# Kernel tuning notes

Measured on AMD Instinct MI355X. Metric: run time of the kernel, lower is better.

Reference implementation:

```python
import jax, jax.numpy as jnp
import numpy as np

D = 128        # node_state_dim
F = 10         # len(CHOSEN_CONNECTION_FEATURES)
N_IP = 20000
N_CONN = 100000
E = 200000
T = 3


def _seg_mean(vals, ids, n):
    s = jax.ops.segment_sum(vals, ids, num_segments=n)
    c = jax.ops.segment_sum(jnp.ones((vals.shape[0], 1), vals.dtype), ids, num_segments=n)
    return s / jnp.maximum(c, 1.0)


def _gru(x, h, kernel, rec_kernel, bias):
    # keras GRUCell, reset_after=True, gate order [z, r, hh]
    xm = x @ kernel + bias[0]
    hm = h @ rec_kernel + bias[1]
    xz, xr, xh = jnp.split(xm, 3, axis=-1)
    hz, hr, hh = jnp.split(hm, 3, axis=-1)
    z = jax.nn.sigmoid(xz + hz)
    r = jax.nn.sigmoid(xr + hr)
    hcand = jnp.tanh(xh + r * hh)
    return z * h + (1.0 - z) * hcand


def setup_inputs() -> dict:
    key = jax.random.key(0)
    ks = jax.random.split(key, 24)
    s = 0.02
    inp = {
        "feature_connection": jax.random.normal(ks[0], (N_CONN, F), jnp.float32),
        "src_ip_to_connection": jax.random.randint(ks[1], (E,), 0, N_IP, jnp.int32),
        "dst_ip_to_connection": jax.random.randint(ks[2], (E,), 0, N_CONN, jnp.int32),
        "src_connection_to_ip": jax.random.randint(ks[3], (E,), 0, N_CONN, jnp.int32),
        "dst_connection_to_ip": jax.random.randint(ks[4], (E,), 0, N_IP, jnp.int32),
        # message MLPs
        "W_m1": jax.random.normal(ks[5], (2 * D, D), jnp.float32) * s,
        "b_m1": jnp.zeros((D,), jnp.float32),
        "W_m2": jax.random.normal(ks[6], (2 * D, D), jnp.float32) * s,
        "b_m2": jnp.zeros((D,), jnp.float32),
        # GRU cells
        "gru_ip_k": jax.random.normal(ks[7], (D, 3 * D), jnp.float32) * s,
        "gru_ip_r": jax.random.normal(ks[8], (D, 3 * D), jnp.float32) * s,
        "gru_ip_b": jnp.zeros((2, 3 * D), jnp.float32),
        "gru_c_k": jax.random.normal(ks[9], (D, 3 * D), jnp.float32) * s,
        "gru_c_r": jax.random.normal(ks[10], (D, 3 * D), jnp.float32) * s,
        "gru_c_b": jnp.zeros((2, 3 * D), jnp.float32),
        # readout MLP
        "W_r1": jax.random.normal(ks[11], (D, 128), jnp.float32) * s,
        "b_r1": jnp.zeros((128,), jnp.float32),
        "W_r2": jax.random.normal(ks[12], (128, 64), jnp.float32) * s,
        "b_r2": jnp.zeros((64,), jnp.float32),
        "W_r3": jax.random.normal(ks[13], (64, 15), jnp.float32) * s,
        "b_r3": jnp.zeros((15,), jnp.float32),
    }
    return inp


def reference(feature_connection, src_ip_to_connection, dst_ip_to_connection,
              src_connection_to_ip, dst_connection_to_ip,
              W_m1, b_m1, W_m2, b_m2,
              gru_ip_k, gru_ip_r, gru_ip_b,
              gru_c_k, gru_c_r, gru_c_b,
              W_r1, b_r1, W_r2, b_r2, W_r3, b_r3):
    ip_state = jnp.ones((N_IP, D), jnp.float32)
    connection_state = jnp.concatenate(
        [feature_connection, jnp.zeros((N_CONN, D - F), jnp.float32)], axis=1)

    for _ in range(T):
        # ip -> connection messages
        nn_in = jnp.concatenate([ip_state[src_ip_to_connection],
                                 connection_state[dst_ip_to_connection]], axis=1)
        ip_message = jax.nn.relu(nn_in @ W_m1 + b_m1)            # [E, D]
        ip_mean = _seg_mean(ip_message, dst_ip_to_connection, N_CONN)
        # connection -> ip messages
        nn_in2 = jnp.concatenate([connection_state[src_connection_to_ip],
                                  ip_state[dst_connection_to_ip]], axis=1)
        conn_message = jax.nn.relu(nn_in2 @ W_m2 + b_m2)         # [E, D]
        conn_mean = _seg_mean(conn_message, dst_connection_to_ip, N_IP)
        # GRU updates
        ip_state = _gru(conn_mean, ip_state, gru_ip_k, gru_ip_r, gru_ip_b)
        connection_state = _gru(ip_mean, connection_state, gru_c_k, gru_c_r, gru_c_b)

    h = jax.nn.relu(connection_state @ W_r1 + b_r1)
    h = jax.nn.relu(h @ W_r2 + b_r2)
    return jax.nn.softmax(h @ W_r3 + b_r3, axis=-1)              # [N_CONN, 15]
```

## Files before the change

### kernel.cpp

```cpp
#include <hip/hip_runtime.h>
#include <math.h>

#define D 128
#define NF 10
#define N_IP 20000
#define N_CONN 100000
#define NE 200000
#define T_ROUNDS 3

typedef unsigned short u16;
using bf16x8 = __attribute__((ext_vector_type(8))) short;
using floatx4 = __attribute__((ext_vector_type(4))) float;

__device__ inline u16 f2bf(float f) {
  union { float f; unsigned u; } v; v.f = f;
  unsigned u = v.u;
  return (u16)((u + 0x7fffu + ((u >> 16) & 1u)) >> 16);
}
__device__ inline float bf2f(u16 h) {
  union { unsigned u; float f; } v; v.u = ((unsigned)h) << 16; return v.f;
}

__device__ inline float fsigmoid(float s) { return 1.f / (1.f + __expf(-s)); }
__device__ inline float ftanh(float a) {
  a = fminf(fmaxf(a, -15.f), 15.f);
  float e = __expf(2.f * a);
  return (e - 1.f) / (e + 1.f);
}

__device__ __forceinline__ void gld16(const u16* g, u16* l) {
  __builtin_amdgcn_global_load_lds(
      (const __attribute__((address_space(1))) unsigned int*)g,
      (__attribute__((address_space(3))) unsigned int*)l, 16, 0, 0);
}

__global__ void k_init_all(u16* __restrict__ ip_state, u16* __restrict__ conn_state,
                           const float* __restrict__ feat, int* __restrict__ cnt) {
  int i = blockIdx.x * blockDim.x + threadIdx.x;
  const int nip = N_IP * D;
  const int nstate = (N_IP + N_CONN) * D;
  if (i < nip) {
    ip_state[i] = 0x3F80;
  } else if (i < nstate) {
    int j = i - nip;
    int r = j >> 7, c = j & 127;
    conn_state[j] = (c < NF) ? f2bf(feat[r * NF + c]) : (u16)0;
  }
  if (i < N_CONN + N_IP) cnt[i] = 0;
}

__global__ void k_prep_all(
    const float* __restrict__ gik, const float* __restrict__ gir,
    const float* __restrict__ gck, const float* __restrict__ gcr,
    const float* __restrict__ Wm1, const float* __restrict__ Wm2,
    const float* __restrict__ Wr1, const float* __restrict__ Wr2,
    u16* __restrict__ gikb, u16* __restrict__ girb,
    u16* __restrict__ gckb, u16* __restrict__ gcrb,
    u16* __restrict__ wm1b, u16* __restrict__ wm2b,
    u16* __restrict__ wm1t, u16* __restrict__ wm2t,
    u16* __restrict__ wr1b, u16* __restrict__ wr2b, float* __restrict__ csum) {
  int i = blockIdx.x * blockDim.x + threadIdx.x;
  if (i < 196608) {
    int m = i / 49152, r = i % 49152;
    const float* W = (m == 0) ? gik : (m == 1) ? gir : (m == 2) ? gck : gcr;
    u16* Wb = (m == 0) ? gikb : (m == 1) ? girb : (m == 2) ? gckb : gcrb;
    int col = r >> 7, k = r & 127;
    Wb[r] = f2bf(W[k * 384 + col]);
  } else if (i < 278528) {
    int j = i - 196608;
    int m = j / 16384, r = j % 16384;
    const float* W; u16* Wb; int k0;
    if (m == 0) { W = Wm1; Wb = wm1b; k0 = 128; }
    else if (m == 1) { W = Wm2; Wb = wm2b; k0 = 128; }
    else if (m == 2) { W = Wm1; Wb = wm1t; k0 = 0; }
    else if (m == 3) { W = Wm2; Wb = wm2t; k0 = 0; }
    else { W = Wr1; Wb = wr1b; k0 = 0; }
    int col = r >> 7, k = r & 127;
    Wb[r] = f2bf(W[(k0 + k) * 128 + col]);
  } else if (i < 286720) {
    int r = i - 278528;
    int col = r >> 7, k = r & 127;
    wr2b[r] = f2bf(Wr2[k * 64 + col]);
  } else if (i < 286848) {
    int c = i - 286720;
    float s = 0.f;
    for (int k = 0; k < 128; k++) s += Wm1[k * 128 + c];
    csum[c] = s;
  }
}

__global__ void k_initP_count(const float* __restrict__ csum, const float* __restrict__ feat,
                              const float* __restrict__ Wm2,
                              u16* __restrict__ P1, u16* __restrict__ P2,
                              const int* __restrict__ d1, const int* __restrict__ d2,
                              int* __restrict__ c1, int* __restrict__ c2) {
  int i = blockIdx.x * blockDim.x + threadIdx.x;
  if (i < NE) {
    atomicAdd(&c1[d1[i]], 1);
    atomicAdd(&c2[d2[i]], 1);
  }
  const int n1 = N_IP * 16;
  const int n2 = N_CONN * 16;
  if (i < n1) {
    int r = i >> 4, g = i & 15;
    u16 v[8];
#pragma unroll
    for (int k = 0; k < 8; k++) v[k] = f2bf(csum[g * 8 + k]);
    *(uint4*)(P1 + (size_t)r * 128 + g * 8) = *(const uint4*)v;
  } else if (i < n1 + n2) {
    int j = i - n1;
    int r = j >> 4, g = j & 15;
    float acc[8] = {0.f, 0.f, 0.f, 0.f, 0.f, 0.f, 0.f, 0.f};
#pragma unroll
    for (int k = 0; k < NF; k++) {
      float f = feat[(size_t)r * NF + k];
      const float* wrow = Wm2 + (size_t)k * 128 + g * 8;
#pragma unroll
      for (int c = 0; c < 8; c++) acc[c] += f * wrow[c];
    }
    u16 v[8];
#pragma unroll
    for (int c = 0; c < 8; c++) v[c] = f2bf(acc[c]);
    *(uint4*)(P2 + (size_t)r * 128 + g * 8) = *(const uint4*)v;
  }
}

__global__ void k_scan_part2(const int* __restrict__ cnt1, int* __restrict__ bsum1,
                             int n1, int nb1,
                             const int* __restrict__ cnt2, int* __restrict__ bsum2, int n2) {
  const int* cnt; int* bsum; int n, b;
  if ((int)blockIdx.x < nb1) { cnt = cnt1; bsum = bsum1; n = n1; b = blockIdx.x; }
  else { cnt = cnt2; bsum = bsum2; n = n2; b = blockIdx.x - nb1; }
  int t = threadIdx.x;
  int base = b * 1024 + t * 4;
  int s = 0;
#pragma unroll
  for (int i = 0; i < 4; i++) { int j = base + i; if (j < n) s += cnt[j]; }
  for (int d = 32; d > 0; d >>= 1) s += __shfl_xor(s, d, 64);
  __shared__ int wred[4];
  int lane = t & 63, wv = t >> 6;
  if (lane == 0) wred[wv] = s;
  __syncthreads();
  if (t == 0) bsum[b] = wred[0] + wred[1] + wred[2] + wred[3];
}

__device__ inline void scan_mid_body(int* bsum, int m, int t) {
  int v = (t < m) ? bsum[t] : 0;
  int lane = t & 63, wv = t >> 6;
  int x = v;
  for (int d = 1; d < 64; d <<= 1) { int y = __shfl_up(x, d, 64); if (lane >= d) x += y; }
  __shared__ int wsum[4];
  if (lane == 63) wsum[wv] = x;
  __syncthreads();
  int add = 0;
  for (int i = 0; i < wv; i++) add += wsum[i];
  int ex = add + x - v;
  if (t < m) bsum[t] = ex;
  __syncthreads();
}

__global__ void k_scan_mid2(int* __restrict__ bsum1, int m1, int* __restrict__ bsum2, int m2) {
  int t = threadIdx.x;
  scan_mid_body(bsum1, m1, t);
  scan_mid_body(bsum2, m2, t);
}

__global__ void k_scan_final2(const int* __restrict__ cnt1, const int* __restrict__ bsum1,
                              int* __restrict__ off1, int* __restrict__ cur1, int n1, int nb1,
                              const int* __restrict__ cnt2, const int* __restrict__ bsum2,
                              int* __restrict__ off2, int* __restrict__ cur2, int n2) {
  const int* cnt; const int* bsum; int* off; int* cur; int n, b;
  if ((int)blockIdx.x < nb1) {
    cnt = cnt1; bsum = bsum1; off = off1; cur = cur1; n = n1; b = blockIdx.x;
  } else {
    cnt = cnt2; bsum = bsum2; off = off2; cur = cur2; n = n2; b = blockIdx.x - nb1;
  }
  int t = threadIdx.x;
  int base = b * 1024 + t * 4;
  int vals[4]; int s = 0;
#pragma unroll
  for (int i = 0; i < 4; i++) {
    int j = base + i;
    vals[i] = (j < n) ? cnt[j] : 0;
    s += vals[i];
  }
  int lane = t & 63, wv = t >> 6;
  int x = s;
  for (int d = 1; d < 64; d <<= 1) { int y = __shfl_up(x, d, 64); if (lane >= d) x += y; }
  __shared__ int wsum[4];
  if (lane == 63) wsum[wv] = x;
  __syncthreads();
  int add = 0;
  for (int i = 0; i < wv; i++) add += wsum[i];
  int run = add + x - s + bsum[b];
#pragma unroll
  for (int i = 0; i < 4; i++) {
    int j = base + i;
    if (j < n) { off[j] = run; cur[j] = run; }
    run += vals[i];
  }
}

__global__ void k_scatter(const int* __restrict__ s1, const int* __restrict__ d1,
                          const int* __restrict__ s2, const int* __restrict__ d2,
                          int* __restrict__ cur1, int* __restrict__ cur2,
                          int* __restrict__ o1, int* __restrict__ o2) {
  int e = blockIdx.x * blockDim.x + threadIdx.x;
  if (e >= NE) return;
  int p1 = atomicAdd(&cur1[d1[e]], 1);
  o1[p1] = s1[e];
  int p2 = atomicAdd(&cur2[d2[e]], 1);
  o2[p2] = s2[e];
}

__global__ __launch_bounds__(256, 4) void k_msggru(
    u16* __restrict__ st1, const u16* __restrict__ wq1, const float* __restrict__ qb1,
    const u16* __restrict__ P1g, const int* __restrict__ srcs1g,
    const int* __restrict__ off1g, const int* __restrict__ cnt1g,
    const u16* __restrict__ wx1, const u16* __restrict__ wh1, const float* __restrict__ gb1,
    const u16* __restrict__ wp1, u16* __restrict__ Pn1, int r1, int tiles1,
    u16* __restrict__ st2, const u16* __restrict__ wq2, const float* __restrict__ qb2,
    const u16* __restrict__ P2g, const int* __restrict__ srcs2g,
    const int* __restrict__ off2g, const int* __restrict__ cnt2g,
    const u16* __restrict__ wx2, const u16* __restrict__ wh2, const float* __restrict__ gb2,
    const u16* __restrict__ wp2, u16* __restrict__ Pn2, int r2, int doP) {
  __shared__ __align__(16) char smem[40960];
  u16* Wls = (u16*)smem;
  u16* Qb = (u16*)smem;
  u16* bufA = (u16*)smem;
  u16* bufB = (u16*)(smem + 12288);
  u16* Hls = (u16*)(smem + 24576);
  int* offLs = (int*)(smem + 24064);
  int* cntLs = (int*)(smem + 24320);
  u16* H; const u16* Wqb; const float* qbias; const u16* P;
  const int* srcs; const int* off; const int* cnt;
  const u16* Wxb; const u16* Whb; const float* gbias;
  const u16* Wpt; u16* Pn; int rows, bm;
  if ((int)blockIdx.x < tiles1) {
    H = st1; Wqb = wq1; qbias = qb1; P = P1g; srcs = srcs1g; off = off1g; cnt = cnt1g;
    Wxb = wx1; Whb = wh1; gbias = gb1; Wpt = wp1; Pn = Pn1; rows = r1; bm = blockIdx.x * 64;
  } else {
    H = st2; Wqb = wq2; qbias = qb2; P = P2g; srcs = srcs2g; off = off2g; cnt = cnt2g;
    Wxb = wx2; Whb = wh2; gbias = gb2; Wpt = wp2; Pn = Pn2; rows = r2;
    bm = (blockIdx.x - tiles1) * 64;
  }
  const int tid = threadIdx.x, wv = tid >> 6, lane = tid & 63;
  const int lrow = lane & 15, quad = lane >> 4;
  const int slot = lane & 15;
  const int rowl = wv * 4 + (lane >> 4);
#pragma unroll
  for (int i = 0; i < 4; i++)
    gld16(Wqb + (size_t)(i * 16 + rowl) * 128 + ((slot ^ rowl) * 8),
          Wls + (size_t)(i * 16 + wv * 4) * 128 + lane * 8);
#pragma unroll
  for (int i = 0; i < 4; i++)
    gld16(H + (size_t)(bm + i * 16 + rowl) * 128 + ((slot ^ rowl) * 8),
          Hls + (size_t)(i * 16 + wv * 4) * 128 + lane * 8);
  if (tid < 64) {
    int node = bm + tid;
    offLs[tid] = (node < rows) ? off[node] : 0;
    cntLs[tid] = (node < rows) ? cnt[node] : 0;
  }
  __syncthreads();
  bf16x8 ah[4];
#pragma unroll
  for (int ks = 0; ks < 4; ks++)
    ah[ks] = *(const bf16x8*)(Hls + (size_t)(wv * 16 + lrow) * 128 + (((ks * 4 + quad) ^ lrow) * 8));
  floatx4 acc[8];
#pragma unroll
  for (int ct = 0; ct < 8; ct++) acc[ct] = {0.f, 0.f, 0.f, 0.f};
#pragma unroll
  for (int ks = 0; ks < 4; ks++) {
#pragma unroll
    for (int j = 0; j < 4; j++) {
      bf16x8 b = *(const bf16x8*)(Wls + (size_t)(j * 16 + lrow) * 128 + (((4 * ks + quad) ^ lrow) * 8));
      acc[j] = __builtin_amdgcn_mfma_f32_16x16x32_bf16(ah[ks], b, acc[j], 0, 0, 0);
    }
  }
  __syncthreads();
#pragma unroll
  for (int i = 0; i < 4; i++)
    gld16(Wqb + (size_t)(64 + i * 16 + rowl) * 128 + ((slot ^ rowl) * 8),
          Wls + (size_t)(i * 16 + wv * 4) * 128 + lane * 8);
  __syncthreads();
#pragma unroll
  for (int ks = 0; ks < 4; ks++) {
#pragma unroll
    for (int j = 0; j < 4; j++) {
      bf16x8 b = *(const bf16x8*)(Wls + (size_t)(j * 16 + lrow) * 128 + (((4 * ks + quad) ^ lrow) * 8));
      acc[4 + j] = __builtin_amdgcn_mfma_f32_16x16x32_bf16(ah[ks], b, acc[4 + j], 0, 0, 0);
    }
  }
  __syncthreads();
#pragma unroll
  for (int ct = 0; ct < 8; ct++) {
    int col = ct * 16 + lrow;
    float bv = qbias[col];
#pragma unroll
    for (int reg = 0; reg < 4; reg++) {
      int lr = wv * 16 + quad * 4 + reg;
      Qb[(size_t)lr * 128 + col] = f2bf(acc[ct][reg] + bv);
    }
  }
  __syncthreads();
#pragma unroll
  for (int it = 0; it < 4; it++) {
    int task = it * 256 + tid;
    int nl = task >> 4, g = task & 15;
    int node = bm + nl;
    if (node >= rows) continue;
    int c8 = g << 3;
    float q[8];
    {
      uint4 qv = *(const uint4*)(Qb + (size_t)nl * 128 + c8);
      unsigned qq[4] = {qv.x, qv.y, qv.z, qv.w};
#pragma unroll
      for (int k = 0; k < 4; k++) {
        q[2 * k] = __uint_as_float(qq[k] << 16);
        q[2 * k + 1] = __uint_as_float(qq[k] & 0xffff0000u);
      }
    }
    float acg[8] = {0.f, 0.f, 0.f, 0.f, 0.f, 0.f, 0.f, 0.f};
    int o = offLs[nl], n = cntLs[nl];
    int i = 0;
    for (; i + 4 <= n; i += 4) {
      int s0 = srcs[o + i], s1 = srcs[o + i + 1], s2 = srcs[o + i + 2], s3 = srcs[o + i + 3];
      uint4 v0 = *(const uint4*)(P + (size_t)s0 * 128 + c8);
      uint4 v1 = *(const uint4*)(P + (size_t)s1 * 128 + c8);
      uint4 v2 = *(const uint4*)(P + (size_t)s2 * 128 + c8);
      uint4 v3 = *(const uint4*)(P + (size_t)s3 * 128 + c8);
      unsigned w[16] = {v0.x, v0.y, v0.z, v0.w, v1.x, v1.y, v1.z, v1.w,
                        v2.x, v2.y, v2.z, v2.w, v3.x, v3.y, v3.z, v3.w};
#pragma unroll
      for (int e = 0; e < 4; e++)
#pragma unroll
        for (int k = 0; k < 4; k++) {
          unsigned ww = w[e * 4 + k];
          float lo = __uint_as_float(ww << 16);
          float hi = __uint_as_float(ww & 0xffff0000u);
          acg[2 * k] += fmaxf(lo + q[2 * k], 0.f);
          acg[2 * k + 1] += fmaxf(hi + q[2 * k + 1], 0.f);
        }
    }
    for (; i < n; i++) {
      int s0 = srcs[o + i];
      uint4 v0 = *(const uint4*)(P + (size_t)s0 * 128 + c8);
      unsigned w[4] = {v0.x, v0.y, v0.z, v0.w};
#pragma unroll
      for (int k = 0; k < 4; k++) {
        unsigned ww = w[k];
        float lo = __uint_as_float(ww << 16);
        float hi = __uint_as_float(ww & 0xffff0000u);
        acg[2 * k] += fmaxf(lo + q[2 * k], 0.f);
        acg[2 * k + 1] += fmaxf(hi + q[2 * k + 1], 0.f);
      }
    }
    float inv = 1.f / fmaxf((float)n, 1.f);
    bf16x8 ov;
#pragma unroll
    for (int k = 0; k < 8; k++) ov[k] = (short)f2bf(acg[k] * inv);
    *(bf16x8*)(Qb + (size_t)nl * 128 + ((g ^ (nl & 15)) * 8)) = ov;
  }
  __syncthreads();
  bf16x8 ax[4];
#pragma unroll
  for (int ks = 0; ks < 4; ks++)
    ax[ks] = *(const bf16x8*)(Qb + (size_t)(wv * 16 + lrow) * 128 + (((ks * 4 + quad) ^ lrow) * 8));
  const int lr0 = wv * 16 + quad * 4;
  __syncthreads();
#pragma unroll
  for (int j = 0; j < 3; j++)
    gld16(Wxb + (size_t)(j * 128 + 0 * 16 + rowl) * 128 + ((slot ^ rowl) * 8),
          bufA + (size_t)(j * 16 + wv * 4) * 128 + lane * 8);
  for (int ch = 0; ch < 8; ch++) {
    __syncthreads();
#pragma unroll
    for (int j = 0; j < 3; j++)
      gld16(Whb + (size_t)(j * 128 + ch * 16 + rowl) * 128 + ((slot ^ rowl) * 8),
            bufB + (size_t)(j * 16 + wv * 4) * 128 + lane * 8);
    floatx4 gacc[3][2];
#pragma unroll
    for (int g = 0; g < 3; g++) {
      gacc[g][0] = {0.f, 0.f, 0.f, 0.f};
      gacc[g][1] = {0.f, 0.f, 0.f, 0.f};
    }
#pragma unroll
    for (int ks = 0; ks < 4; ks++) {
      int posu = ((4 * ks + quad) ^ lrow) * 8;
#pragma unroll
      for (int g = 0; g < 3; g++) {
        bf16x8 bx = *(const bf16x8*)(bufA + (size_t)(g * 16 + lrow) * 128 + posu);
        gacc[g][0] = __builtin_amdgcn_mfma_f32_16x16x32_bf16(ax[ks], bx, gacc[g][0], 0, 0, 0);
      }
    }
    __syncthreads();
    if (ch < 7) {
#pragma unroll
      for (int j = 0; j < 3; j++)
        gld16(Wxb + (size_t)(j * 128 + (ch + 1) * 16 + rowl) * 128 + ((slot ^ rowl) * 8),
              bufA + (size_t)(j * 16 + wv * 4) * 128 + lane * 8);
    }
#pragma unroll
    for (int ks = 0; ks < 4; ks++) {
      int posu = ((4 * ks + quad) ^ lrow) * 8;
#pragma unroll
      for (int g = 0; g < 3; g++) {
        bf16x8 bh = *(const bf16x8*)(bufB + (size_t)(g * 16 + lrow) * 128 + posu);
        gacc[g][1] = __builtin_amdgcn_mfma_f32_16x16x32_bf16(ah[ks], bh, gacc[g][1], 0, 0, 0);
      }
    }
    int hcol = ch * 16 + lrow;
    float bxz = gbias[hcol];
    float bxr = gbias[128 + hcol];
    float bxh = gbias[256 + hcol];
    float bhz = gbias[384 + hcol];
    float bhr = gbias[384 + 128 + hcol];
    float bhh = gbias[384 + 256 + hcol];
    int ggr = 2 * ch + (lrow >> 3);
    int gel = lrow & 7;
#pragma unroll
    for (int reg = 0; reg < 4; reg++) {
      int lr = lr0 + reg;
      float xz = gacc[0][0][reg] + bxz;
      float xr = gacc[1][0][reg] + bxr;
      float xh = gacc[2][0][reg] + bxh;
      float hz = gacc[0][1][reg] + bhz;
      float hr = gacc[1][1][reg] + bhr;
      float hh = gacc[2][1][reg] + bhh;
      float z = fsigmoid(xz + hz);
      float rr = fsigmoid(xr + hr);
      float hc = ftanh(xh + rr * hh);
      u16* hp = Hls + (size_t)lr * 128 + ((ggr ^ (lr & 15)) * 8) + gel;
      float hold = bf2f(*hp);
      *hp = f2bf(z * hold + (1.f - z) * hc);
    }
  }
  __syncthreads();
#pragma unroll
  for (int i = 0; i < 4; i++) {
    int task = i * 256 + tid;
    int row = task >> 4, g = task & 15;
    int grow = bm + row;
    if (grow < rows)
      *(uint4*)(H + (size_t)grow * 128 + g * 8) =
          *(const uint4*)(Hls + (size_t)row * 128 + ((g ^ (row & 15)) * 8));
  }
  if (!doP) return;
  bf16x8 ah2[4];
#pragma unroll
  for (int ks = 0; ks < 4; ks++)
    ah2[ks] = *(const bf16x8*)(Hls + (size_t)(wv * 16 + lrow) * 128 + (((ks * 4 + quad) ^ lrow) * 8));
#pragma unroll
  for (int i = 0; i < 4; i++)
    gld16(Wpt + (size_t)(i * 16 + rowl) * 128 + ((slot ^ rowl) * 8),
          Wls + (size_t)(i * 16 + wv * 4) * 128 + lane * 8);
  __syncthreads();
#pragma unroll
  for (int ct = 0; ct < 8; ct++) acc[ct] = {0.f, 0.f, 0.f, 0.f};
#pragma unroll
  for (int ks = 0; ks < 4; ks++) {
#pragma unroll
    for (int j = 0; j < 4; j++) {
      bf16x8 b = *(const bf16x8*)(Wls + (size_t)(j * 16 + lrow) * 128 + (((4 * ks + quad) ^ lrow) * 8));
      acc[j] = __builtin_amdgcn_mfma_f32_16x16x32_bf16(ah2[ks], b, acc[j], 0, 0, 0);
    }
  }
  __syncthreads();
#pragma unroll
  for (int i = 0; i < 4; i++)
    gld16(Wpt + (size_t)(64 + i * 16 + rowl) * 128 + ((slot ^ rowl) * 8),
          Wls + (size_t)(i * 16 + wv * 4) * 128 + lane * 8);
  __syncthreads();
#pragma unroll
  for (int ks = 0; ks < 4; ks++) {
#pragma unroll
    for (int j = 0; j < 4; j++) {
      bf16x8 b = *(const bf16x8*)(Wls + (size_t)(j * 16 + lrow) * 128 + (((4 * ks + quad) ^ lrow) * 8));
      acc[4 + j] = __builtin_amdgcn_mfma_f32_16x16x32_bf16(ah2[ks], b, acc[4 + j], 0, 0, 0);
    }
  }
  u16* Cls = Hls;
#pragma unroll
  for (int ct = 0; ct < 8; ct++) {
    int col = ct * 16 + lrow;
#pragma unroll
    for (int reg = 0; reg < 4; reg++) {
      int lr = wv * 16 + quad * 4 + reg;
      Cls[(size_t)lr * 128 + col] = f2bf(acc[ct][reg]);
    }
  }
  __syncthreads();
#pragma unroll
  for (int i = 0; i < 4; i++) {
    int task = i * 256 + tid;
    int row = task >> 4, g = task & 15;
    int grow = bm + row;
    if (grow < rows)
      *(uint4*)(Pn + (size_t)grow * 128 + g * 8) =
          *(const uint4*)(Cls + (size_t)row * 128 + g * 8);
  }
}

__global__ __launch_bounds__(256, 4) void k_readout2(
    const u16* __restrict__ S, const u16* __restrict__ W1b, const float* __restrict__ b1,
    const u16* __restrict__ W2b, const float* __restrict__ b2,
    const float* __restrict__ W3, const float* __restrict__ b3,
    float* __restrict__ out, int M) {
  __shared__ __align__(16) char smem[33792];
  u16* Wls = (u16*)smem;
  u16* H1ls = (u16*)smem;
  u16* W2ls = (u16*)(smem + 17408);
  u16* H2ls = (u16*)smem;
  float* W3ls = (float*)(smem + 9216);
  float* b3ls = (float*)(smem + 9216 + 3840);
  const int tid = threadIdx.x, wv = tid >> 6, lane = tid & 63;
  const int lrow = lane & 15, quad = lane >> 4;
  const int slot = lane & 15;
  const int rowl = wv * 4 + (lane >> 4);
  const int bm = blockIdx.x * 64;
#pragma unroll
  for (int i = 0; i < 8; i++)
    gld16(W1b + (size_t)(i * 16 + rowl) * 128 + ((slot ^ rowl) * 8),
          Wls + (size_t)(i * 16 + wv * 4) * 128 + lane * 8);
  const int arow = bm + wv * 16 + lrow;
  const bool arv = arow < M;
  const bf16x8 zv = {0, 0, 0, 0, 0, 0, 0, 0};
  bf16x8 a[4];
#pragma unroll
  for (int ks = 0; ks < 4; ks++)
    a[ks] = arv ? *(const bf16x8*)(S + (size_t)arow * 128 + quad * 8 + ks * 32) : zv;
  __syncthreads();
  floatx4 acc1[8];
#pragma unroll
  for (int ct = 0; ct < 8; ct++) acc1[ct] = {0.f, 0.f, 0.f, 0.f};
#pragma unroll
  for (int ks = 0; ks < 4; ks++) {
#pragma unroll
    for (int ct = 0; ct < 8; ct++) {
      bf16x8 b = *(const bf16x8*)(Wls + (size_t)(ct * 16 + lrow) * 128 + (((4 * ks + quad) ^ lrow) * 8));
      acc1[ct] = __builtin_amdgcn_mfma_f32_16x16x32_bf16(a[ks], b, acc1[ct], 0, 0, 0);
    }
  }
  __syncthreads();
#pragma unroll
  for (int ct = 0; ct < 8; ct++) {
    int col = ct * 16 + lrow;
    float bv = b1[col];
#pragma unroll
    for (int reg = 0; reg < 4; reg++) {
      int lr = wv * 16 + quad * 4 + reg;
      H1ls[(size_t)lr * 136 + col] = f2bf(fmaxf(acc1[ct][reg] + bv, 0.f));
    }
  }
#pragma unroll
  for (int i = 0; i < 4; i++)
    gld16(W2b + (size_t)(i * 16 + rowl) * 128 + ((slot ^ rowl) * 8),
          W2ls + (size_t)(i * 16 + wv * 4) * 128 + lane * 8);
  __syncthreads();
  bf16x8 a2[4];
#pragma unroll
  for (int ks = 0; ks < 4; ks++)
    a2[ks] = *(const bf16x8*)(H1ls + (size_t)(wv * 16 + lrow) * 136 + quad * 8 + ks * 32);
  floatx4 acc2[4];
#pragma unroll
  for (int ct = 0; ct < 4; ct++) acc2[ct] = {0.f, 0.f, 0.f, 0.f};
#pragma unroll
  for (int ks = 0; ks < 4; ks++) {
#pragma unroll
    for (int ct = 0; ct < 4; ct++) {
      bf16x8 b = *(const bf16x8*)(W2ls + (size_t)(ct * 16 + lrow) * 128 + (((4 * ks + quad) ^ lrow) * 8));
      acc2[ct] = __builtin_amdgcn_mfma_f32_16x16x32_bf16(a2[ks], b, acc2[ct], 0, 0, 0);
    }
  }
  __syncthreads();
#pragma unroll
  for (int ct = 0; ct < 4; ct++) {
    int col = ct * 16 + lrow;
    float bv = b2[col];
#pragma unroll
    for (int reg = 0; reg < 4; reg++) {
      int lr = wv * 16 + quad * 4 + reg;
      H2ls[(size_t)lr * 72 + col] = f2bf(fmaxf(acc2[ct][reg] + bv, 0.f));
    }
  }
  for (int l = tid; l < 960; l += 256) W3ls[l] = W3[l];
  if (tid < 15) b3ls[tid] = b3[tid];
  __syncthreads();
  {
    int col = tid & 15;
    int rb = (tid >> 4) * 4;
    float lg[4] = {0.f, 0.f, 0.f, 0.f};
    if (col < 15) {
      float b3v = b3ls[col];
      lg[0] = b3v; lg[1] = b3v; lg[2] = b3v; lg[3] = b3v;
      for (int k = 0; k < 64; k++) {
        float w = W3ls[k * 15 + col];
#pragma unroll
        for (int r = 0; r < 4; r++)
          lg[r] += bf2f(H2ls[(size_t)(rb + r) * 72 + k]) * w;
      }
    }
#pragma unroll
    for (int r = 0; r < 4; r++) {
      float v = (col < 15) ? lg[r] : -3.0e38f;
      float m = v;
#pragma unroll
      for (int d = 1; d < 16; d <<= 1) m = fmaxf(m, __shfl_xor(m, d, 16));
      float e = (col < 15) ? __expf(lg[r] - m) : 0.f;
      float s = e;
#pragma unroll
      for (int d = 1; d < 16; d <<= 1) s += __shfl_xor(s, d, 16);
      int gr2 = bm + rb + r;
      if (col < 15 && gr2 < M) out[(size_t)gr2 * 15 + col] = e / s;
    }
  }
}

extern "C" void kernel_launch(void* const* d_in, const int* in_sizes, int n_in,
                              void* d_out, int out_size, void* d_ws, size_t ws_size,
                              hipStream_t stream) {
  const float* feat = (const float*)d_in[0];
  const int* src1 = (const int*)d_in[1];
  const int* dst1 = (const int*)d_in[2];
  const int* src2 = (const int*)d_in[3];
  const int* dst2 = (const int*)d_in[4];
  const float* Wm1 = (const float*)d_in[5];
  const float* bm1 = (const float*)d_in[6];
  const float* Wm2 = (const float*)d_in[7];
  const float* bm2 = (const float*)d_in[8];
  const float* gik = (const float*)d_in[9];
  const float* gir = (const float*)d_in[10];
  const float* gib = (const float*)d_in[11];
  const float* gck = (const float*)d_in[12];
  const float* gcr = (const float*)d_in[13];
  const float* gcb = (const float*)d_in[14];
  const float* Wr1 = (const float*)d_in[15];
  const float* br1 = (const float*)d_in[16];
  const float* Wr2 = (const float*)d_in[17];
  const float* br2 = (const float*)d_in[18];
  const float* Wr3 = (const float*)d_in[19];
  const float* br3 = (const float*)d_in[20];
  float* out = (float*)d_out;

  u16* w16 = (u16*)d_ws;
  size_t o = 0;
  u16* ip_state = w16 + o;   o += (size_t)N_IP * D;
  u16* conn_state = w16 + o; o += (size_t)N_CONN * D;
  u16* P1a = w16 + o;        o += (size_t)N_IP * D;
  u16* P2a = w16 + o;        o += (size_t)N_CONN * D;
  u16* P1b = w16 + o;        o += (size_t)N_IP * D;
  u16* P2b = w16 + o;        o += (size_t)N_CONN * D;
  u16* gikb = w16 + o;       o += 49152;
  u16* girb = w16 + o;       o += 49152;
  u16* gckb = w16 + o;       o += 49152;
  u16* gcrb = w16 + o;       o += 49152;
  u16* wm1b = w16 + o;       o += 16384;
  u16* wm2b = w16 + o;       o += 16384;
  u16* wm1t = w16 + o;       o += 16384;
  u16* wm2t = w16 + o;       o += 16384;
  u16* wr1b = w16 + o;       o += 16384;
  u16* wr2b = w16 + o;       o += 8192;
  float* csum = (float*)(w16 + o); o += 256;
  int* ip = (int*)(w16 + o);
  int* cnt1 = ip;  ip += N_CONN;
  int* cnt2 = ip;  ip += N_IP;
  int* off1 = ip;  ip += N_CONN;
  int* off2 = ip;  ip += N_IP;
  int* cur1 = ip;  ip += N_CONN;
  int* cur2 = ip;  ip += N_IP;
  int* srcs1 = ip; ip += NE;
  int* srcs2 = ip; ip += NE;
  int* bsum1 = ip; ip += 256;
  int* bsum2 = ip; ip += 256;

  const int BT = 256;

  const int nstate = (N_IP + N_CONN) * D;
  k_init_all<<<(nstate + BT - 1) / BT, BT, 0, stream>>>(ip_state, conn_state, feat, cnt1);
  k_prep_all<<<(286848 + BT - 1) / BT, BT, 0, stream>>>(
      gik, gir, gck, gcr, Wm1, Wm2, Wr1, Wr2,
      gikb, girb, gckb, gcrb, wm1b, wm2b, wm1t, wm2t, wr1b, wr2b, csum);
  const int nPinit = (N_IP + N_CONN) * 16;
  k_initP_count<<<(nPinit + BT - 1) / BT, BT, 0, stream>>>(
      csum, feat, Wm2, P1a, P2a, dst1, dst2, cnt1, cnt2);

  const int nb1 = (N_CONN + 1023) / 1024, nb2 = (N_IP + 1023) / 1024;
  k_scan_part2<<<nb1 + nb2, 256, 0, stream>>>(cnt1, bsum1, N_CONN, nb1, cnt2, bsum2, N_IP);
  k_scan_mid2<<<1, 256, 0, stream>>>(bsum1, nb1, bsum2, nb2);
  k_scan_final2<<<nb1 + nb2, 256, 0, stream>>>(cnt1, bsum1, off1, cur1, N_CONN, nb1,
                                               cnt2, bsum2, off2, cur2, N_IP);
  k_scatter<<<(NE + BT - 1) / BT, BT, 0, stream>>>(src1, dst1, src2, dst2,
                                                   cur1, cur2, srcs1, srcs2);

  const int t64ip = (N_IP + 63) / 64;
  const int t64cn = (N_CONN + 63) / 64;

  u16* P1buf[2] = {P1a, P1b};
  u16* P2buf[2] = {P2a, P2b};
  for (int t = 0; t < T_ROUNDS; t++) {
    int cu = t & 1, nx = cu ^ 1;
    k_msggru<<<t64ip + t64cn, 256, 0, stream>>>(
        ip_state, wm2b, bm2, P2buf[cu], srcs2, off2, cnt2, gikb, girb, gib,
        wm1t, P1buf[nx], N_IP, t64ip,
        conn_state, wm1b, bm1, P1buf[cu], srcs1, off1, cnt1, gckb, gcrb, gcb,
        wm2t, P2buf[nx], N_CONN, (t < T_ROUNDS - 1) ? 1 : 0);
  }

  k_readout2<<<t64cn, 256, 0, stream>>>(conn_state, wr1b, br1, wr2b, br2,
                                        Wr3, br3, out, N_CONN);
}
```

Measured before the change: 447.4 us.

## Enlarge msggru tiles to 128 rows with 512-thread blocks and predicated gather

The fused message+GRU kernel now processes 128 nodes per block with 8 waves instead of 64 nodes with 4 waves. Each staged weight chunk in LDS is therefore reused across twice as many rows. Per-node offset and count are now held in registers instead of LDS. The gather loop handles the remainder through predication instead of a scalar tail loop, and the readout logits loop reads H2 eight values at a time. The larger LDS footprint (64KB) and block size reduce occupancy and may cut the number of resident blocks per CU.

```diff
diff --git a/kernel.cpp b/kernel.cpp
--- a/kernel.cpp
+++ b/kernel.cpp
@@ -213,7 +213,7 @@
   o2[p2] = s2[e];
 }
 
-__global__ __launch_bounds__(256, 4) void k_msggru(
+__global__ __launch_bounds__(512, 4) void k_msggru(
     u16* __restrict__ st1, const u16* __restrict__ wq1, const float* __restrict__ qb1,
     const u16* __restrict__ P1g, const int* __restrict__ srcs1g,
     const int* __restrict__ off1g, const int* __restrict__ cnt1g,
@@ -224,42 +224,45 @@
     const int* __restrict__ off2g, const int* __restrict__ cnt2g,
     const u16* __restrict__ wx2, const u16* __restrict__ wh2, const float* __restrict__ gb2,
     const u16* __restrict__ wp2, u16* __restrict__ Pn2, int r2, int doP) {
-  __shared__ __align__(16) char smem[40960];
+  __shared__ __align__(16) char smem[65536];
   u16* Wls = (u16*)smem;
   u16* Qb = (u16*)smem;
   u16* bufA = (u16*)smem;
   u16* bufB = (u16*)(smem + 12288);
-  u16* Hls = (u16*)(smem + 24576);
-  int* offLs = (int*)(smem + 24064);
-  int* cntLs = (int*)(smem + 24320);
+  u16* Hls = (u16*)(smem + 32768);
   u16* H; const u16* Wqb; const float* qbias; const u16* P;
   const int* srcs; const int* off; const int* cnt;
   const u16* Wxb; const u16* Whb; const float* gbias;
   const u16* Wpt; u16* Pn; int rows, bm;
   if ((int)blockIdx.x < tiles1) {
     H = st1; Wqb = wq1; qbias = qb1; P = P1g; srcs = srcs1g; off = off1g; cnt = cnt1g;
-    Wxb = wx1; Whb = wh1; gbias = gb1; Wpt = wp1; Pn = Pn1; rows = r1; bm = blockIdx.x * 64;
+    Wxb = wx1; Whb = wh1; gbias = gb1; Wpt = wp1; Pn = Pn1; rows = r1; bm = blockIdx.x * 128;
   } else {
     H = st2; Wqb = wq2; qbias = qb2; P = P2g; srcs = srcs2g; off = off2g; cnt = cnt2g;
     Wxb = wx2; Whb = wh2; gbias = gb2; Wpt = wp2; Pn = Pn2; rows = r2;
-    bm = (blockIdx.x - tiles1) * 64;
+    bm = (blockIdx.x - tiles1) * 128;
   }
   const int tid = threadIdx.x, wv = tid >> 6, lane = tid & 63;
   const int lrow = lane & 15, quad = lane >> 4;
-  const int slot = lane & 15;
-  const int rowl = wv * 4 + (lane >> 4);
-#pragma unroll
-  for (int i = 0; i < 4; i++)
-    gld16(Wqb + (size_t)(i * 16 + rowl) * 128 + ((slot ^ rowl) * 8),
-          Wls + (size_t)(i * 16 + wv * 4) * 128 + lane * 8);
-#pragma unroll
-  for (int i = 0; i < 4; i++)
-    gld16(H + (size_t)(bm + i * 16 + rowl) * 128 + ((slot ^ rowl) * 8),
-          Hls + (size_t)(i * 16 + wv * 4) * 128 + lane * 8);
-  if (tid < 64) {
-    int node = bm + tid;
-    offLs[tid] = (node < rows) ? off[node] : 0;
-    cntLs[tid] = (node < rows) ? cnt[node] : 0;
+#pragma unroll
+  for (int j = 0; j < 2; j++) {
+    int c = j * 512 + tid;
+    int row = c >> 4, sl = c & 15;
+    gld16(Wqb + (size_t)row * 128 + ((sl ^ (row & 15)) * 8), Wls + (size_t)c * 8);
+  }
+#pragma unroll
+  for (int i = 0; i < 4; i++) {
+    int c = i * 512 + tid;
+    int row = c >> 4, sl = c & 15;
+    gld16(H + (size_t)(bm + row) * 128 + ((sl ^ (row & 15)) * 8), Hls + (size_t)c * 8);
+  }
+  int oArr[4], nArr[4];
+#pragma unroll
+  for (int it = 0; it < 4; it++) {
+    int nl = (it * 512 + tid) >> 4;
+    int node = bm + nl;
+    oArr[it] = (node < rows) ? off[node] : 0;
+    nArr[it] = (node < rows) ? cnt[node] : 0;
   }
   __syncthreads();
   bf16x8 ah[4];
@@ -279,9 +282,11 @@
   }
   __syncthreads();
 #pragma unroll
-  for (int i = 0; i < 4; i++)
-    gld16(Wqb + (size_t)(64 + i * 16 + rowl) * 128 + ((slot ^ rowl) * 8),
-          Wls + (size_t)(i * 16 + wv * 4) * 128 + lane * 8);
+  for (int j = 0; j < 2; j++) {
+    int c = j * 512 + tid;
+    int row = c >> 4, sl = c & 15;
+    gld16(Wqb + (size_t)(64 + row) * 128 + ((sl ^ (row & 15)) * 8), Wls + (size_t)c * 8);
+  }
   __syncthreads();
 #pragma unroll
   for (int ks = 0; ks < 4; ks++) {
@@ -305,7 +310,7 @@
   __syncthreads();
 #pragma unroll
   for (int it = 0; it < 4; it++) {
-    int task = it * 256 + tid;
+    int task = it * 512 + tid;
     int nl = task >> 4, g = task & 15;
     int node = bm + nl;
     if (node >= rows) continue;
@@ -321,10 +326,13 @@
       }
     }
     float acg[8] = {0.f, 0.f, 0.f, 0.f, 0.f, 0.f, 0.f, 0.f};
-    int o = offLs[nl], n = cntLs[nl];
-    int i = 0;
-    for (; i + 4 <= n; i += 4) {
-      int s0 = srcs[o + i], s1 = srcs[o + i + 1], s2 = srcs[o + i + 2], s3 = srcs[o + i + 3];
+    int o = oArr[it], n = nArr[it];
+    for (int i = 0; i < n; i += 4) {
+      int rem = n - i;
+      int s0 = srcs[o + i];
+      int s1 = srcs[o + i + (rem > 1 ? 1 : 0)];
+      int s2 = srcs[o + i + (rem > 2 ? 2 : 0)];
+      int s3 = srcs[o + i + (rem > 3 ? 3 : 0)];
       uint4 v0 = *(const uint4*)(P + (size_t)s0 * 128 + c8);
       uint4 v1 = *(const uint4*)(P + (size_t)s1 * 128 + c8);
       uint4 v2 = *(const uint4*)(P + (size_t)s2 * 128 + c8);
@@ -332,27 +340,17 @@
       unsigned w[16] = {v0.x, v0.y, v0.z, v0.w, v1.x, v1.y, v1.z, v1.w,
                         v2.x, v2.y, v2.z, v2.w, v3.x, v3.y, v3.z, v3.w};
 #pragma unroll
-      for (int e = 0; e < 4; e++)
+      for (int e = 0; e < 4; e++) {
+        bool val = (e == 0) || (rem > e);
 #pragma unroll
         for (int k = 0; k < 4; k++) {
           unsigned ww = w[e * 4 + k];
           float lo = __uint_as_float(ww << 16);
           float hi = __uint_as_float(ww & 0xffff0000u);
-          acg[2 * k] += fmaxf(lo + q[2 * k], 0.f);
-          acg[2 * k + 1] += fmaxf(hi + q[2 * k + 1], 0.f);
+          float t0 = fmaxf(lo + q[2 * k], 0.f);
+          float t1 = fmaxf(hi + q[2 * k + 1], 0.f);
+          if (val) { acg[2 * k] += t0; acg[2 * k + 1] += t1; }
         }
-    }
-    for (; i < n; i++) {
-      int s0 = srcs[o + i];
-      uint4 v0 = *(const uint4*)(P + (size_t)s0 * 128 + c8);
-      unsigned w[4] = {v0.x, v0.y, v0.z, v0.w};
-#pragma unroll
-      for (int k = 0; k < 4; k++) {
-        unsigned ww = w[k];
-        float lo = __uint_as_float(ww << 16);
-        float hi = __uint_as_float(ww & 0xffff0000u);
-        acg[2 * k] += fmaxf(lo + q[2 * k], 0.f);
-        acg[2 * k + 1] += fmaxf(hi + q[2 * k + 1], 0.f);
       }
     }
     float inv = 1.f / fmaxf((float)n, 1.f);
@@ -369,15 +367,25 @@
   const int lr0 = wv * 16 + quad * 4;
   __syncthreads();
 #pragma unroll
-  for (int j = 0; j < 3; j++)
-    gld16(Wxb + (size_t)(j * 128 + 0 * 16 + rowl) * 128 + ((slot ^ rowl) * 8),
-          bufA + (size_t)(j * 16 + wv * 4) * 128 + lane * 8);
+  for (int j = 0; j < 2; j++) {
+    int c = j * 512 + tid;
+    if (c < 768) {
+      int gate = c >> 8, colw = (c >> 4) & 15, sl = c & 15;
+      gld16(Wxb + (size_t)(gate * 128 + 0 * 16 + colw) * 128 + ((sl ^ colw) * 8),
+            bufA + (size_t)c * 8);
+    }
+  }
   for (int ch = 0; ch < 8; ch++) {
     __syncthreads();
 #pragma unroll
-    for (int j = 0; j < 3; j++)
-      gld16(Whb + (size_t)(j * 128 + ch * 16 + rowl) * 128 + ((slot ^ rowl) * 8),
-            bufB + (size_t)(j * 16 + wv * 4) * 128 + lane * 8);
+    for (int j = 0; j < 2; j++) {
+      int c = j * 512 + tid;
+      if (c < 768) {
+        int gate = c >> 8, colw = (c >> 4) & 15, sl = c & 15;
+        gld16(Whb + (size_t)(gate * 128 + ch * 16 + colw) * 128 + ((sl ^ colw) * 8),
+              bufB + (size_t)c * 8);
+      }
+    }
     floatx4 gacc[3][2];
 #pragma unroll
     for (int g = 0; g < 3; g++) {
@@ -396,9 +404,14 @@
     __syncthreads();
     if (ch < 7) {
 #pragma unroll
-      for (int j = 0; j < 3; j++)
-        gld16(Wxb + (size_t)(j * 128 + (ch + 1) * 16 + rowl) * 128 + ((slot ^ rowl) * 8),
-              bufA + (size_t)(j * 16 + wv * 4) * 128 + lane * 8);
+      for (int j = 0; j < 2; j++) {
+        int c = j * 512 + tid;
+        if (c < 768) {
+          int gate = c >> 8, colw = (c >> 4) & 15, sl = c & 15;
+          gld16(Wxb + (size_t)(gate * 128 + (ch + 1) * 16 + colw) * 128 + ((sl ^ colw) * 8),
+                bufA + (size_t)c * 8);
+        }
+      }
     }
 #pragma unroll
     for (int ks = 0; ks < 4; ks++) {
@@ -438,8 +451,8 @@
   __syncthreads();
 #pragma unroll
   for (int i = 0; i < 4; i++) {
-    int task = i * 256 + tid;
-    int row = task >> 4, g = task & 15;
+    int c = i * 512 + tid;
+    int row = c >> 4, g = c & 15;
     int grow = bm + row;
     if (grow < rows)
       *(uint4*)(H + (size_t)grow * 128 + g * 8) =
@@ -451,9 +464,11 @@
   for (int ks = 0; ks < 4; ks++)
     ah2[ks] = *(const bf16x8*)(Hls + (size_t)(wv * 16 + lrow) * 128 + (((ks * 4 + quad) ^ lrow) * 8));
 #pragma unroll
-  for (int i = 0; i < 4; i++)
-    gld16(Wpt + (size_t)(i * 16 + rowl) * 128 + ((slot ^ rowl) * 8),
-          Wls + (size_t)(i * 16 + wv * 4) * 128 + lane * 8);
+  for (int j = 0; j < 2; j++) {
+    int c = j * 512 + tid;
+    int row = c >> 4, sl = c & 15;
+    gld16(Wpt + (size_t)row * 128 + ((sl ^ (row & 15)) * 8), Wls + (size_t)c * 8);
+  }
   __syncthreads();
 #pragma unroll
   for (int ct = 0; ct < 8; ct++) acc[ct] = {0.f, 0.f, 0.f, 0.f};
@@ -467,9 +482,11 @@
   }
   __syncthreads();
 #pragma unroll
-  for (int i = 0; i < 4; i++)
-    gld16(Wpt + (size_t)(64 + i * 16 + rowl) * 128 + ((slot ^ rowl) * 8),
-          Wls + (size_t)(i * 16 + wv * 4) * 128 + lane * 8);
+  for (int j = 0; j < 2; j++) {
+    int c = j * 512 + tid;
+    int row = c >> 4, sl = c & 15;
+    gld16(Wpt + (size_t)(64 + row) * 128 + ((sl ^ (row & 15)) * 8), Wls + (size_t)c * 8);
+  }
   __syncthreads();
 #pragma unroll
   for (int ks = 0; ks < 4; ks++) {
@@ -492,8 +509,8 @@
   __syncthreads();
 #pragma unroll
   for (int i = 0; i < 4; i++) {
-    int task = i * 256 + tid;
-    int row = task >> 4, g = task & 15;
+    int c = i * 512 + tid;
+    int row = c >> 4, g = c & 15;
     int grow = bm + row;
     if (grow < rows)
       *(uint4*)(Pn + (size_t)grow * 128 + g * 8) =
@@ -593,11 +610,16 @@
     if (col < 15) {
       float b3v = b3ls[col];
       lg[0] = b3v; lg[1] = b3v; lg[2] = b3v; lg[3] = b3v;
-      for (int k = 0; k < 64; k++) {
-        float w = W3ls[k * 15 + col];
-#pragma unroll
-        for (int r = 0; r < 4; r++)
-          lg[r] += bf2f(H2ls[(size_t)(rb + r) * 72 + k]) * w;
+      for (int k8 = 0; k8 < 64; k8 += 8) {
+        float w[8];
+#pragma unroll
+        for (int j = 0; j < 8; j++) w[j] = W3ls[(k8 + j) * 15 + col];
+#pragma unroll
+        for (int r = 0; r < 4; r++) {
+          bf16x8 hv = *(const bf16x8*)(H2ls + (size_t)(rb + r) * 72 + k8);
+#pragma unroll
+          for (int j = 0; j < 8; j++) lg[r] += bf2f((u16)hv[j]) * w[j];
+        }
       }
     }
 #pragma unroll
@@ -692,16 +714,17 @@
   k_scatter<<<(NE + BT - 1) / BT, BT, 0, stream>>>(src1, dst1, src2, dst2,
                                                    cur1, cur2, srcs1, srcs2);
 
-  const int t64ip = (N_IP + 63) / 64;
+  const int t128ip = (N_IP + 127) / 128;
+  const int t128cn = (N_CONN + 127) / 128;
   const int t64cn = (N_CONN + 63) / 64;
 
   u16* P1buf[2] = {P1a, P1b};
   u16* P2buf[2] = {P2a, P2b};
   for (int t = 0; t < T_ROUNDS; t++) {
     int cu = t & 1, nx = cu ^ 1;
-    k_msggru<<<t64ip + t64cn, 256, 0, stream>>>(
+    k_msggru<<<t128ip + t128cn, 512, 0, stream>>>(
         ip_state, wm2b, bm2, P2buf[cu], srcs2, off2, cnt2, gikb, girb, gib,
-        wm1t, P1buf[nx], N_IP, t64ip,
+        wm1t, P1buf[nx], N_IP, t128ip,
         conn_state, wm1b, bm1, P1buf[cu], srcs1, off1, cnt1, gckb, gcrb, gcb,
         wm2t, P2buf[nx], N_CONN, (t < T_ROUNDS - 1) ? 1 : 0);
   }
```

Result: no change. 455.2 us (+1.8%).
